# Kernel optimization log

Hardware: AMD Instinct MI355X
Metric: run time of the kernel (lower is better)

## Reference

```python
import jax, jax.numpy as jnp
import numpy as np

B = 2
SPATIAL = (480, 360, 32)  # cylindrical grid (rho, phi, z) as in Cylinder3D
N = 400000
C = 32
EPS = 1e-5
NEG_SLOPE = 0.01
OFFSETS = [(d0, d2) for d0 in (-1, 0, 1) for d2 in (-1, 0, 1)]  # kernel (3,1,3)


def setup_inputs() -> dict:
    key = jax.random.key(0)
    k1, k2 = jax.random.split(key)
    # unique active voxel coordinates: sample unique linear indices then decode
    total = B * SPATIAL[0] * SPATIAL[1] * SPATIAL[2]
    rng = np.random.default_rng(0)
    lin = rng.choice(total, size=N, replace=False).astype(np.int64)
    b = lin // (SPATIAL[0] * SPATIAL[1] * SPATIAL[2])
    r = lin % (SPATIAL[0] * SPATIAL[1] * SPATIAL[2])
    c0 = r // (SPATIAL[1] * SPATIAL[2])
    r = r % (SPATIAL[1] * SPATIAL[2])
    c1 = r // SPATIAL[2]
    c2 = r % SPATIAL[2]
    coords = jnp.asarray(np.stack([b, c0, c1, c2], axis=1), dtype=jnp.int32)
    features = jax.random.normal(k1, (N, C), dtype=jnp.float32)
    weight = jax.random.normal(k2, (9, C, C), dtype=jnp.float32) * (1.0 / np.sqrt(9 * C))
    gamma = jnp.ones((C,), dtype=jnp.float32)
    beta = jnp.zeros((C,), dtype=jnp.float32)
    return {"features": features, "coords": coords, "weight": weight,
            "gamma": gamma, "beta": beta}


def _subm_conv(features, coords, weight):
    n = features.shape[0]
    # dense coordinate -> row-index lookup table (rulebook hash)
    lookup = jnp.full((B,) + SPATIAL, -1, dtype=jnp.int32)
    lookup = lookup.at[coords[:, 0], coords[:, 1], coords[:, 2], coords[:, 3]].set(
        jnp.arange(n, dtype=jnp.int32))
    out = jnp.zeros((n, weight.shape[-1]), dtype=features.dtype)
    for k, (d0, d2) in enumerate(OFFSETS):
        n0 = coords[:, 1] + d0
        n2 = coords[:, 3] + d2
        valid = (n0 >= 0) & (n0 < SPATIAL[0]) & (n2 >= 0) & (n2 < SPATIAL[2])
        nbr = lookup[coords[:, 0],
                     jnp.clip(n0, 0, SPATIAL[0] - 1),
                     coords[:, 2],
                     jnp.clip(n2, 0, SPATIAL[2] - 1)]
        nbr = jnp.where(valid, nbr, -1)
        # gather (masked) -> GEMM -> accumulate (scatter to same active sites)
        gathered = jnp.where((nbr >= 0)[:, None],
                             features[jnp.clip(nbr, 0)], 0.0)
        out = out + gathered @ weight[k]
    return out


def reference(features, coords, weight, gamma, beta):
    x = _subm_conv(features, coords, weight)          # [N, C]
    x = jnp.where(x >= 0, x, NEG_SLOPE * x)           # LeakyReLU (before BN per forward)
    mean = jnp.mean(x, axis=0)                        # BatchNorm1d, training mode
    var = jnp.mean((x - mean) ** 2, axis=0)           # biased variance
    y = (x - mean) * jax.lax.rsqrt(var + EPS) * gamma + beta
    return y
```

## Files before the change

kernel.cpp:

```cpp
#include <hip/hip_runtime.h>
#include <hip/hip_bf16.h>

#define S0 480
#define S1 360
#define S2 32
#define SLAB (S1 * S2)
#define CH 32
#define EPS 1e-5f
#define SLOPE 0.01f

#define NCOL (2 * S0 * S1)
#define SCAN_BLKS (NCOL / 256)

typedef short short8 __attribute__((ext_vector_type(8)));
typedef float f32x16 __attribute__((ext_vector_type(16)));

__device__ __forceinline__ unsigned short f2b(float f) {
    union { __hip_bfloat16 b; unsigned short u; } v;
    v.b = __float2bfloat16(f);
    return v.u;
}

__global__ __launch_bounds__(256) void clear_mask_k(uint4* __restrict__ mask)
{
    int i = blockIdx.x * 256 + threadIdx.x;
    if (i < NCOL / 4) mask[i] = make_uint4(0u, 0u, 0u, 0u);
}

__global__ __launch_bounds__(256) void scatter_or_k(
    const int4* __restrict__ coords, unsigned int* __restrict__ mask, int n)
{
    int i = blockIdx.x * 256 + threadIdx.x;
    if (i < n) {
        int4 c = coords[i];
        int col = (c.x * S0 + c.y) * S1 + c.z;
        atomicOr(&mask[col], 1u << c.w);
    }
}

__global__ __launch_bounds__(256) void scanA_k(
    const unsigned int* __restrict__ mask, int* __restrict__ bsum,
    const float* __restrict__ weight, short8* __restrict__ bfrag)
{
    int t = threadIdx.x;
    int pc = __popc(mask[blockIdx.x * 256 + t]);
#pragma unroll
    for (int m = 32; m > 0; m >>= 1) pc += __shfl_xor(pc, m, 64);
    __shared__ int red[4];
    if ((t & 63) == 0) red[t >> 6] = pc;
    __syncthreads();
    if (t == 0) bsum[blockIdx.x] = red[0] + red[1] + red[2] + red[3];

    if (blockIdx.x == 0 && t < 64) {
        int half = t >> 5;
        int col  = t & 31;
#pragma unroll
        for (int k = 0; k < 9; ++k)
#pragma unroll
            for (int h = 0; h < 2; ++h) {
                short8 fr;
#pragma unroll
                for (int j = 0; j < 8; ++j) {
                    int ic = h * 16 + half * 8 + j;
                    fr[j] = (short)f2b(weight[k * (CH * CH) + ic * CH + col]);
                }
                bfrag[(k * 2 + h) * 64 + t] = fr;
            }
    }
}

__global__ __launch_bounds__(256) void scanBC_k(
    const unsigned int* __restrict__ mask, const int* __restrict__ bsum,
    uint2* __restrict__ tab)
{
    int t = threadIdx.x;
    int b = blockIdx.x;

    int partial = 0;
    for (int j = t; j < b; j += 256) partial += bsum[j];
#pragma unroll
    for (int m = 32; m > 0; m >>= 1) partial += __shfl_xor(partial, m, 64);
    __shared__ int red[4];
    if ((t & 63) == 0) red[t >> 6] = partial;
    __syncthreads();
    int base = red[0] + red[1] + red[2] + red[3];

    int col = b * 256 + t;
    unsigned int m = mask[col];
    int pc = __popc(m);
    __shared__ int sa[256], sb[256];
    sa[t] = pc; __syncthreads();
    int* src = sa; int* dst = sb;
#pragma unroll
    for (int off = 1; off < 256; off <<= 1) {
        dst[t] = src[t] + (t >= off ? src[t - off] : 0);
        __syncthreads();
        int* tmp = src; src = dst; dst = tmp;
    }
    int excl = src[t] - pc + base;
    tab[col] = make_uint2(m, (unsigned int)excl);
}

__global__ __launch_bounds__(256) void rank_k(
    const int4*  __restrict__ coords,
    const uint2* __restrict__ tab,
    uint2*       __restrict__ pinfo,
    int*         __restrict__ rankof,
    int n)
{
    int i = blockIdx.x * 256 + threadIdx.x;
    if (i >= n) return;
    int4 c = coords[i];
    int col = (c.x * S0 + c.y) * S1 + c.z;
    int lin = col * 32 + c.w;
    uint2 tv = tab[col];
    int rank = (int)tv.y + __popc(tv.x & ((1u << c.w) - 1u));
    pinfo[rank] = make_uint2((unsigned int)i, (unsigned int)lin);
    rankof[i] = rank;
}

__global__ __launch_bounds__(256) void pack_k(
    const float* __restrict__ features,
    const uint2* __restrict__ pinfo,
    unsigned short* __restrict__ featb,
    int n)
{
    int t = threadIdx.x;
    int row = blockIdx.x * 32 + (t >> 3);
    int j = t & 7;
    if (row >= n) return;
    unsigned int orig = pinfo[row].x;
    float4 f = ((const float4*)(features + (size_t)orig * CH))[j];
    ushort4 u;
    u.x = f2b(f.x); u.y = f2b(f.y); u.z = f2b(f.z); u.w = f2b(f.w);
    ((ushort4*)(featb + (size_t)row * CH))[j] = u;
}

__global__ __launch_bounds__(256) void conv_sorted_k(
    const unsigned short* __restrict__ featb,
    const uint2* __restrict__ pinfo,
    const uint2* __restrict__ tab,
    const short8* __restrict__ bfrag,
    unsigned short* __restrict__ xout,
    float*        __restrict__ stats_part,
    int n, int ntile)
{
    int nwg = gridDim.x;
    int bid = blockIdx.x;
    int q = nwg >> 3, r = nwg & 7;
    int xcd = bid & 7, sidx = bid >> 3;
    int blk = (xcd < r ? xcd * (q + 1) : r * (q + 1) + (xcd - r) * q) + sidx;

    int tid  = threadIdx.x;
    int lane = tid & 63;
    int wv   = tid >> 6;
    int half = lane >> 5;
    int col  = lane & 31;

    short8 B[9][2];
#pragma unroll
    for (int t = 0; t < 9; ++t) {
        B[t][0] = bfrag[(t * 2 + 0) * 64 + lane];
        B[t][1] = bfrag[(t * 2 + 1) * 64 + lane];
    }

    int tile = blk * 4 + wv;
    bool tlive = (tile < ntile);
    int p  = tile * 32 + col;
    bool live = tlive && (p < n);
    int pc = live ? p : 0;

    uint2 pi = pinfo[pc];
    int lin = (int)pi.y;
    int c2 = lin & 31;
    int colv = lin >> 5;
    int c0 = (lin / SLAB) % S0;

    int nbr[9];
#pragma unroll
    for (int d0 = 0; d0 < 3; ++d0) {
        int n0 = c0 + d0 - 1;
        bool v0 = (n0 >= 0) & (n0 < S0) & live;
        uint2 tv = v0 ? tab[colv + (d0 - 1) * S1] : make_uint2(0u, 0u);
#pragma unroll
        for (int d2 = 0; d2 < 3; ++d2) {
            int n2 = c2 + d2 - 1;
            int rk = -1;
            if (v0 && n2 >= 0 && n2 < S2 && ((tv.x >> n2) & 1u))
                rk = (int)tv.y + __popc(tv.x & ((1u << n2) - 1u));
            nbr[d0 * 3 + d2] = rk;
        }
    }

    bool act[9];
#pragma unroll
    for (int t = 0; t < 9; ++t) act[t] = (__any(nbr[t] >= 0) != 0);

    short8 A0[9], A1[9];
#pragma unroll
    for (int t = 0; t < 9; ++t) {
        short8 z;
#pragma unroll
        for (int j = 0; j < 8; ++j) z[j] = 0;
        A0[t] = z; A1[t] = z;
        int nb = nbr[t];
        if (nb >= 0) {
            const short* fp = (const short*)featb + (size_t)nb * CH;
            A0[t] = *(const short8*)(fp + half * 8);
            A1[t] = *(const short8*)(fp + 16 + half * 8);
        }
    }

    f32x16 acc;
#pragma unroll
    for (int i = 0; i < 16; ++i) acc[i] = 0.f;
#pragma unroll
    for (int t = 0; t < 9; ++t) {
        if (act[t]) {
            acc = __builtin_amdgcn_mfma_f32_32x32x16_bf16(A0[t], B[t][0], acc, 0, 0, 0);
            acc = __builtin_amdgcn_mfma_f32_32x32x16_bf16(A1[t], B[t][1], acc, 0, 0, 0);
        }
    }

    float s = 0.f, qq = 0.f;
#pragma unroll
    for (int i = 0; i < 16; ++i) {
        float v = acc[i];
        v = v >= 0.f ? v : SLOPE * v;
        int row = (i & 3) + 8 * (i >> 2) + 4 * half;
        int prow = tile * 32 + row;
        if (tlive && prow < n) {
            xout[(size_t)prow * CH + col] = f2b(v);
            s += v; qq += v * v;
        }
    }

    s  += __shfl_xor(s, 32);
    qq += __shfl_xor(qq, 32);

    __shared__ float lsum[4][32];
    __shared__ float lsq[4][32];
    if (lane < 32) { lsum[wv][col] = s; lsq[wv][col] = qq; }
    __syncthreads();
    if (tid < 32) {
        stats_part[(size_t)bid * 64 + tid] =
            lsum[0][tid] + lsum[1][tid] + lsum[2][tid] + lsum[3][tid];
    } else if (tid < 64) {
        int cc = tid - 32;
        stats_part[(size_t)bid * 64 + tid] =
            lsq[0][cc] + lsq[1][cc] + lsq[2][cc] + lsq[3][cc];
    }
}

__global__ __launch_bounds__(256) void reduce_stats_k(
    const float* __restrict__ part, float* __restrict__ stats, int nb)
{
    int c = blockIdx.x;
    float s = 0.f;
    for (int i = threadIdx.x; i < nb; i += 256)
        s += part[(size_t)i * 64 + c];
#pragma unroll
    for (int m = 32; m > 0; m >>= 1) s += __shfl_xor(s, m, 64);
    __shared__ float red[4];
    int wv = threadIdx.x >> 6;
    if ((threadIdx.x & 63) == 0) red[wv] = s;
    __syncthreads();
    if (threadIdx.x == 0) stats[c] = red[0] + red[1] + red[2] + red[3];
}

__global__ __launch_bounds__(256) void bn_gather_k(
    const unsigned short* __restrict__ xb,
    const int*   __restrict__ rankof,
    const float* __restrict__ stats,
    const float* __restrict__ gamma,
    const float* __restrict__ beta,
    float* __restrict__ out,
    int n)
{
    int total = n * 4;
    int stride = gridDim.x * blockDim.x;
    int g = blockIdx.x * blockDim.x + threadIdx.x;
    int c8 = g & 3;

    float scale[8], shift[8];
    float rn = 1.0f / (float)n;
#pragma unroll
    for (int j = 0; j < 8; ++j) {
        int oc = c8 * 8 + j;
        float m  = stats[oc] * rn;
        float vv = stats[CH + oc] * rn - m * m;
        float iv = rsqrtf(vv + EPS) * gamma[oc];
        scale[j] = iv;
        shift[j] = beta[oc] - m * iv;
    }

    const short8* x8 = (const short8*)xb;
    for (; g < total; g += stride) {
        int i = g >> 2;
        int rank = rankof[i];
        short8 v = x8[(size_t)rank * 4 + c8];
        float f[8];
#pragma unroll
        for (int j = 0; j < 8; ++j) {
            union { unsigned int u; float f; } w;
            w.u = ((unsigned int)(unsigned short)v[j]) << 16;
            f[j] = fmaf(w.f, scale[j], shift[j]);
        }
        float4* o = (float4*)(out + (size_t)i * CH + c8 * 8);
        o[0] = make_float4(f[0], f[1], f[2], f[3]);
        o[1] = make_float4(f[4], f[5], f[6], f[7]);
    }
}

extern "C" void kernel_launch(void* const* d_in, const int* in_sizes, int n_in,
                              void* d_out, int out_size, void* d_ws, size_t ws_size,
                              hipStream_t stream)
{
    const float* features = (const float*)d_in[0];
    const int4*  coords   = (const int4*)d_in[1];
    const float* weight   = (const float*)d_in[2];
    const float* gamma    = (const float*)d_in[3];
    const float* beta     = (const float*)d_in[4];
    float* out = (float*)d_out;

    int n = in_sizes[0] / CH;
    int ntile = (n + 31) / 32;
    int conv_blocks = (ntile + 3) / 4;

    char* w = (char*)d_ws;
    unsigned int* mask = (unsigned int*)w;  w += (size_t)NCOL * 4;
    uint2* tab = (uint2*)w;                 w += (size_t)NCOL * 8;
    int* bsum = (int*)w;                    w += ((size_t)SCAN_BLKS * 4 + 255) & ~(size_t)255;
    uint2* pinfo = (uint2*)w;               w += (size_t)n * 8;
    int* rankof = (int*)w;                  w += (size_t)n * 4;
    unsigned short* featb = (unsigned short*)w; w += (size_t)n * CH * 2;
    unsigned short* xout = (unsigned short*)w;  w += (size_t)n * CH * 2;
    float* stats_part = (float*)w;          w += (size_t)conv_blocks * 64 * 4;
    short8* bfrag = (short8*)w;             w += 9 * 2 * 64 * sizeof(short8);
    float* stats = (float*)w;

    clear_mask_k<<<(NCOL / 4 + 255) / 256, 256, 0, stream>>>((uint4*)mask);

    scatter_or_k<<<(n + 255) / 256, 256, 0, stream>>>(coords, mask, n);
    scanA_k<<<SCAN_BLKS, 256, 0, stream>>>(mask, bsum, weight, bfrag);
    scanBC_k<<<SCAN_BLKS, 256, 0, stream>>>(mask, bsum, tab);
    rank_k<<<(n + 255) / 256, 256, 0, stream>>>(coords, tab, pinfo, rankof, n);
    pack_k<<<(n + 31) / 32, 256, 0, stream>>>(features, pinfo, featb, n);

    conv_sorted_k<<<conv_blocks, 256, 0, stream>>>(
        featb, pinfo, tab, bfrag, xout, stats_part, n, ntile);

    reduce_stats_k<<<64, 256, 0, stream>>>(stats_part, stats, conv_blocks);

    bn_gather_k<<<2048, 256, 0, stream>>>(xout, rankof, stats, gamma, beta, out, n);
}
```

Measured before the change: 112.4 us.

## Use persistent XCD-partitioned grids for pack and conv kernels

Both pack_k and conv_sorted_k now launch a fixed 2048-block grid. Each XCD takes a contiguous chunk of row tiles, so the featb rows pack writes are read back by conv on the same XCD, keeping neighbour gathers in that XCD's L2. Conv waves loop over a contiguous run of tiles, which spreads the cost of loading the B fragments and shrinks the stats_part buffer. The risks are fewer waves in flight to hide gather latency, and load imbalance if runs do not divide evenly.

```diff
diff --git a/kernel.cpp b/kernel.cpp
--- a/kernel.cpp
+++ b/kernel.cpp
@@ -123,17 +123,27 @@
     const float* __restrict__ features,
     const uint2* __restrict__ pinfo,
     unsigned short* __restrict__ featb,
-    int n)
-{
+    int n, int ntile)
+{
+    int NB  = gridDim.x;
+    int bpx = NB >> 3;
+    int xcd = blockIdx.x & 7;
+    int ibx = blockIdx.x >> 3;
+    int chunk = (ntile + 7) >> 3;
+    int rstart = xcd * chunk * 32;
+    int rend   = min((xcd + 1) * chunk, ntile) * 32;
+    if (rend > n) rend = n;
+
     int t = threadIdx.x;
-    int row = blockIdx.x * 32 + (t >> 3);
     int j = t & 7;
-    if (row >= n) return;
-    unsigned int orig = pinfo[row].x;
-    float4 f = ((const float4*)(features + (size_t)orig * CH))[j];
-    ushort4 u;
-    u.x = f2b(f.x); u.y = f2b(f.y); u.z = f2b(f.z); u.w = f2b(f.w);
-    ((ushort4*)(featb + (size_t)row * CH))[j] = u;
+    int sub = t >> 3;
+    for (int row = rstart + ibx * 32 + sub; row < rend; row += bpx * 32) {
+        unsigned int orig = pinfo[row].x;
+        float4 f = ((const float4*)(features + (size_t)orig * CH))[j];
+        ushort4 u;
+        u.x = f2b(f.x); u.y = f2b(f.y); u.z = f2b(f.z); u.w = f2b(f.w);
+        ((ushort4*)(featb + (size_t)row * CH))[j] = u;
+    }
 }
 
 __global__ __launch_bounds__(256) void conv_sorted_k(
@@ -145,12 +155,6 @@
     float*        __restrict__ stats_part,
     int n, int ntile)
 {
-    int nwg = gridDim.x;
-    int bid = blockIdx.x;
-    int q = nwg >> 3, r = nwg & 7;
-    int xcd = bid & 7, sidx = bid >> 3;
-    int blk = (xcd < r ? xcd * (q + 1) : r * (q + 1) + (xcd - r) * q) + sidx;
-
     int tid  = threadIdx.x;
     int lane = tid & 63;
     int wv   = tid >> 6;
@@ -164,74 +168,87 @@
         B[t][1] = bfrag[(t * 2 + 1) * 64 + lane];
     }
 
-    int tile = blk * 4 + wv;
-    bool tlive = (tile < ntile);
-    int p  = tile * 32 + col;
-    bool live = tlive && (p < n);
-    int pc = live ? p : 0;
-
-    uint2 pi = pinfo[pc];
-    int lin = (int)pi.y;
-    int c2 = lin & 31;
-    int colv = lin >> 5;
-    int c0 = (lin / SLAB) % S0;
-
-    int nbr[9];
-#pragma unroll
-    for (int d0 = 0; d0 < 3; ++d0) {
-        int n0 = c0 + d0 - 1;
-        bool v0 = (n0 >= 0) & (n0 < S0) & live;
-        uint2 tv = v0 ? tab[colv + (d0 - 1) * S1] : make_uint2(0u, 0u);
-#pragma unroll
-        for (int d2 = 0; d2 < 3; ++d2) {
-            int n2 = c2 + d2 - 1;
-            int rk = -1;
-            if (v0 && n2 >= 0 && n2 < S2 && ((tv.x >> n2) & 1u))
-                rk = (int)tv.y + __popc(tv.x & ((1u << n2) - 1u));
-            nbr[d0 * 3 + d2] = rk;
-        }
-    }
-
-    bool act[9];
-#pragma unroll
-    for (int t = 0; t < 9; ++t) act[t] = (__any(nbr[t] >= 0) != 0);
-
-    short8 A0[9], A1[9];
-#pragma unroll
-    for (int t = 0; t < 9; ++t) {
-        short8 z;
-#pragma unroll
-        for (int j = 0; j < 8; ++j) z[j] = 0;
-        A0[t] = z; A1[t] = z;
-        int nb = nbr[t];
-        if (nb >= 0) {
-            const short* fp = (const short*)featb + (size_t)nb * CH;
-            A0[t] = *(const short8*)(fp + half * 8);
-            A1[t] = *(const short8*)(fp + 16 + half * 8);
-        }
-    }
-
-    f32x16 acc;
-#pragma unroll
-    for (int i = 0; i < 16; ++i) acc[i] = 0.f;
-#pragma unroll
-    for (int t = 0; t < 9; ++t) {
-        if (act[t]) {
-            acc = __builtin_amdgcn_mfma_f32_32x32x16_bf16(A0[t], B[t][0], acc, 0, 0, 0);
-            acc = __builtin_amdgcn_mfma_f32_32x32x16_bf16(A1[t], B[t][1], acc, 0, 0, 0);
-        }
-    }
+    int NB  = gridDim.x;
+    int bpx = NB >> 3;
+    int xcd = blockIdx.x & 7;
+    int ibx = blockIdx.x >> 3;
+    int chunk = (ntile + 7) >> 3;
+    int wpx = bpx * 4;
+    int run = (chunk + wpx - 1) / wpx;
+    int wix = ibx * 4 + wv;
+    int xend = min((xcd + 1) * chunk, ntile);
+    int t0 = xcd * chunk + wix * run;
+    int t1 = min(t0 + run, xend);
 
     float s = 0.f, qq = 0.f;
-#pragma unroll
-    for (int i = 0; i < 16; ++i) {
-        float v = acc[i];
-        v = v >= 0.f ? v : SLOPE * v;
-        int row = (i & 3) + 8 * (i >> 2) + 4 * half;
-        int prow = tile * 32 + row;
-        if (tlive && prow < n) {
-            xout[(size_t)prow * CH + col] = f2b(v);
-            s += v; qq += v * v;
+
+    for (int tile = t0; tile < t1; ++tile) {
+        int p = tile * 32 + col;
+        bool live = (p < n);
+        int pc = live ? p : 0;
+
+        uint2 pi = pinfo[pc];
+        int lin = (int)pi.y;
+        int c2 = lin & 31;
+        int colv = lin >> 5;
+        int c0 = (lin / SLAB) % S0;
+
+        int nbr[9];
+#pragma unroll
+        for (int d0 = 0; d0 < 3; ++d0) {
+            int n0 = c0 + d0 - 1;
+            bool v0 = (n0 >= 0) & (n0 < S0) & live;
+            uint2 tv = v0 ? tab[colv + (d0 - 1) * S1] : make_uint2(0u, 0u);
+#pragma unroll
+            for (int d2 = 0; d2 < 3; ++d2) {
+                int n2 = c2 + d2 - 1;
+                int rk = -1;
+                if (v0 && n2 >= 0 && n2 < S2 && ((tv.x >> n2) & 1u))
+                    rk = (int)tv.y + __popc(tv.x & ((1u << n2) - 1u));
+                nbr[d0 * 3 + d2] = rk;
+            }
+        }
+
+        bool act[9];
+#pragma unroll
+        for (int t = 0; t < 9; ++t) act[t] = (__any(nbr[t] >= 0) != 0);
+
+        short8 A0[9], A1[9];
+#pragma unroll
+        for (int t = 0; t < 9; ++t) {
+            short8 z;
+#pragma unroll
+            for (int j = 0; j < 8; ++j) z[j] = 0;
+            A0[t] = z; A1[t] = z;
+            int nb = nbr[t];
+            if (nb >= 0) {
+                const short* fp = (const short*)featb + (size_t)nb * CH;
+                A0[t] = *(const short8*)(fp + half * 8);
+                A1[t] = *(const short8*)(fp + 16 + half * 8);
+            }
+        }
+
+        f32x16 acc;
+#pragma unroll
+        for (int i = 0; i < 16; ++i) acc[i] = 0.f;
+#pragma unroll
+        for (int t = 0; t < 9; ++t) {
+            if (act[t]) {
+                acc = __builtin_amdgcn_mfma_f32_32x32x16_bf16(A0[t], B[t][0], acc, 0, 0, 0);
+                acc = __builtin_amdgcn_mfma_f32_32x32x16_bf16(A1[t], B[t][1], acc, 0, 0, 0);
+            }
+        }
+
+#pragma unroll
+        for (int i = 0; i < 16; ++i) {
+            float v = acc[i];
+            v = v >= 0.f ? v : SLOPE * v;
+            int row = (i & 3) + 8 * (i >> 2) + 4 * half;
+            int prow = tile * 32 + row;
+            if (prow < n) {
+                xout[(size_t)prow * CH + col] = f2b(v);
+                s += v; qq += v * v;
+            }
         }
     }
 
@@ -243,11 +260,11 @@
     if (lane < 32) { lsum[wv][col] = s; lsq[wv][col] = qq; }
     __syncthreads();
     if (tid < 32) {
-        stats_part[(size_t)bid * 64 + tid] =
+        stats_part[(size_t)blockIdx.x * 64 + tid] =
             lsum[0][tid] + lsum[1][tid] + lsum[2][tid] + lsum[3][tid];
     } else if (tid < 64) {
         int cc = tid - 32;
-        stats_part[(size_t)bid * 64 + tid] =
+        stats_part[(size_t)blockIdx.x * 64 + tid] =
             lsq[0][cc] + lsq[1][cc] + lsq[2][cc] + lsq[3][cc];
     }
 }
@@ -325,7 +342,7 @@
 
     int n = in_sizes[0] / CH;
     int ntile = (n + 31) / 32;
-    int conv_blocks = (ntile + 3) / 4;
+    int conv_blocks = 2048;
 
     char* w = (char*)d_ws;
     unsigned int* mask = (unsigned int*)w;  w += (size_t)NCOL * 4;
@@ -340,12 +357,11 @@
     float* stats = (float*)w;
 
     clear_mask_k<<<(NCOL / 4 + 255) / 256, 256, 0, stream>>>((uint4*)mask);
-
     scatter_or_k<<<(n + 255) / 256, 256, 0, stream>>>(coords, mask, n);
     scanA_k<<<SCAN_BLKS, 256, 0, stream>>>(mask, bsum, weight, bfrag);
     scanBC_k<<<SCAN_BLKS, 256, 0, stream>>>(mask, bsum, tab);
     rank_k<<<(n + 255) / 256, 256, 0, stream>>>(coords, tab, pinfo, rankof, n);
-    pack_k<<<(n + 31) / 32, 256, 0, stream>>>(features, pinfo, featb, n);
+    pack_k<<<2048, 256, 0, stream>>>(features, pinfo, featb, n, ntile);
 
     conv_sorted_k<<<conv_blocks, 256, 0, stream>>>(
         featb, pinfo, tab, bfrag, xout, stats_part, n, ntile);
```

Result: no change. 110.3 us (-1.8%).
